# Kernel optimization log

Hardware: AMD Instinct MI355X
Metric: run time of the kernel (lower is better)

Reference implementation:

```python
import jax, jax.numpy as jnp
import numpy as np

N_NODES = 50000
N_EDGES = 800000
D_MODEL = 128
N_HEADS = 8
HEAD_DIM = D_MODEL // N_HEADS
SCALE = 1.0 / np.sqrt(HEAD_DIM)


def _linear_params(key, d_in, d_out):
    kw, kb = jax.random.split(key)
    bound = 1.0 / np.sqrt(d_in)
    W = jax.random.uniform(kw, (d_in, d_out), jnp.float32, -bound, bound)
    b = jax.random.uniform(kb, (d_out,), jnp.float32, -bound, bound)
    return W, b


def setup_inputs() -> dict:
    key = jax.random.key(0)
    ks = jax.random.split(key, 8)
    node_features = jax.random.normal(ks[0], (N_NODES, D_MODEL), jnp.float32)
    edge_index = jax.random.randint(ks[1], (2, N_EDGES), 0, N_NODES, jnp.int64 if jax.config.jax_enable_x64 else jnp.int32)
    edge_features = jax.random.normal(ks[2], (N_EDGES, D_MODEL), jnp.float32)
    Wq, bq = _linear_params(ks[3], D_MODEL, D_MODEL)
    Wk, bk = _linear_params(ks[4], D_MODEL, D_MODEL)
    Wv, bv = _linear_params(ks[5], D_MODEL, D_MODEL)
    We, be = _linear_params(ks[6], D_MODEL, N_HEADS)
    Wo, bo = _linear_params(ks[7], D_MODEL, D_MODEL)
    return {"node_features": node_features, "edge_index": edge_index,
            "edge_features": edge_features,
            "Wq": Wq, "bq": bq, "Wk": Wk, "bk": bk, "Wv": Wv, "bv": bv,
            "We": We, "be": be, "Wo": Wo, "bo": bo}


def reference(node_features, edge_index, edge_features,
              Wq, bq, Wk, bk, Wv, bv, We, be, Wo, bo):
    N = node_features.shape[0]
    Q = (node_features @ Wq + bq).reshape(N, N_HEADS, HEAD_DIM)
    K = (node_features @ Wk + bk).reshape(N, N_HEADS, HEAD_DIM)
    V = (node_features @ Wv + bv).reshape(N, N_HEADS, HEAD_DIM)
    row, col = edge_index[0], edge_index[1]
    # edge scores: [E, H]
    scores = jnp.einsum('ehd,ehd->eh', Q[row], K[col]) * SCALE
    scores = scores + (edge_features @ We + be)
    # segment softmax over destination node (row), per head
    seg_max = jax.ops.segment_max(scores, row, num_segments=N)          # [N, H]
    seg_max = jnp.where(jnp.isfinite(seg_max), seg_max, 0.0)
    ex = jnp.exp(scores - seg_max[row])                                  # [E, H]
    denom = jax.ops.segment_sum(ex, row, num_segments=N)                 # [N, H]
    att = ex / denom[row]
    # weighted aggregate of neighbor values: [N, H, D]
    out = jax.ops.segment_sum(att[:, :, None] * V[col], row, num_segments=N)
    out = out.reshape(N, D_MODEL)
    return out @ Wo + bo
```

## Files before the change

### kernel.cpp

```cpp
#include <hip/hip_runtime.h>
#include <hip/hip_bf16.h>
#include <math.h>

#define NNODES 50000
#define NEDGES 800000
#define DMODEL 128
#define QK_SCALE 0.25f
#define NSB 196

typedef float fvec4 __attribute__((ext_vector_type(4)));
typedef short sv8  __attribute__((ext_vector_type(8)));

__device__ __forceinline__ unsigned short f2bf(float f) {
    unsigned int u = __float_as_uint(f);
    unsigned int r = (u + 0x7FFFu + ((u >> 16) & 1u)) >> 16;
    return (unsigned short)r;
}

__device__ __forceinline__ void bf8_to_f32(uint4 u, fvec4& lo, fvec4& hi) {
    lo.x = __uint_as_float(u.x << 16); lo.y = __uint_as_float(u.x & 0xFFFF0000u);
    lo.z = __uint_as_float(u.y << 16); lo.w = __uint_as_float(u.y & 0xFFFF0000u);
    hi.x = __uint_as_float(u.z << 16); hi.y = __uint_as_float(u.z & 0xFFFF0000u);
    hi.z = __uint_as_float(u.w << 16); hi.w = __uint_as_float(u.w & 0xFFFF0000u);
}

__global__ __launch_bounds__(256) void prep_kernel(const float* __restrict__ X,
                                                   const float* __restrict__ Wq,
                                                   const float* __restrict__ Wk,
                                                   const float* __restrict__ Wv,
                                                   const float* __restrict__ Wo,
                                                   unsigned short* __restrict__ Xb,
                                                   unsigned short* __restrict__ Wb,
                                                   int* __restrict__ cnt) {
    int i = blockIdx.x * 256 + threadIdx.x;
    if (i < NNODES * 32) {
        float4 v = *(const float4*)&X[(size_t)i * 4];
        ushort4 s;
        s.x = f2bf(v.x); s.y = f2bf(v.y); s.z = f2bf(v.z); s.w = f2bf(v.w);
        *(ushort4*)&Xb[(size_t)i * 4] = s;
    } else {
        int j = i - NNODES * 32;
        if (j < 4 * 16384) {
            int w = j >> 14, rem = j & 16383;
            int n = rem >> 7, k = rem & 127;
            const float* src = (w == 0) ? Wq : (w == 1) ? Wk : (w == 2) ? Wv : Wo;
            Wb[j] = f2bf(src[k * 128 + n]);
        } else {
            int c = j - 4 * 16384;
            if (c < NNODES) cnt[c] = 0;
        }
    }
}

__global__ __launch_bounds__(256) void gemm_qkv(const unsigned short* __restrict__ Xb,
                                                const unsigned short* __restrict__ Wb,
                                                const float* __restrict__ bq,
                                                const float* __restrict__ bk,
                                                const float* __restrict__ bv,
                                                unsigned short* __restrict__ Qb,
                                                unsigned short* __restrict__ KVb,
                                                int M) {
    __shared__ unsigned short Als[64 * 128];
    __shared__ unsigned short Bls[128 * 128];
    char* Ac = (char*)Als;
    char* Bc = (char*)Bls;

    int z = blockIdx.y;
    int r0 = blockIdx.x * 64;
    int tid = threadIdx.x;
    int wave = tid >> 6, lane = tid & 63;

    const char* Wsrc = (const char*)(Wb + (size_t)z * 16384);

    #pragma unroll
    for (int p = 0; p < 4; ++p) {
        int o = p * 4096 + tid * 16;
        int r = o >> 8;
        int gr = r0 + r; if (gr >= M) gr = M - 1;
        uint4 v = *(const uint4*)((const char*)Xb + (size_t)gr * 256 + (o & 255));
        *(uint4*)(Ac + r * 256 + ((o & 255) ^ ((r & 7) << 4))) = v;
    }
    #pragma unroll
    for (int p = 0; p < 8; ++p) {
        int o = p * 4096 + tid * 16;
        int r = o >> 8;
        uint4 v = *(const uint4*)(Wsrc + o);
        *(uint4*)(Bc + (o ^ ((r & 7) << 4))) = v;
    }
    __syncthreads();

    fvec4 acc[8] = {};
    int arow = wave * 16 + (lane & 15);
    int kchunk = (lane >> 4) * 16;

    #pragma unroll
    for (int ks = 0; ks < 4; ++ks) {
        int ain = (ks * 64 + kchunk) ^ ((arow & 7) << 4);
        sv8 af = *(const sv8*)(Ac + arow * 256 + ain);
        #pragma unroll
        for (int cf = 0; cf < 8; ++cf) {
            int brow = cf * 16 + (lane & 15);
            int bin = (ks * 64 + kchunk) ^ ((brow & 7) << 4);
            sv8 bf = *(const sv8*)(Bc + brow * 256 + bin);
            acc[cf] = __builtin_amdgcn_mfma_f32_16x16x32_bf16(af, bf, acc[cf], 0, 0, 0);
        }
    }

    const float* bias = (z == 0) ? bq : (z == 1) ? bk : bv;

    #pragma unroll
    for (int cf = 0; cf < 8; ++cf) {
        int col = cf * 16 + (lane & 15);
        float b = bias[col];
        #pragma unroll
        for (int r = 0; r < 4; ++r) {
            int gr = r0 + wave * 16 + ((lane >> 4) * 4) + r;
            if (gr < M) {
                unsigned short val = f2bf(acc[cf][r] + b);
                if (z == 0) {
                    Qb[(size_t)gr * 128 + col] = val;
                } else {
                    int coff = (z == 1) ? 0 : 128;
                    int off = coff + ((col & 8) << 3) + ((col >> 4) << 3) + (col & 7);
                    KVb[(size_t)gr * 256 + off] = val;
                }
            }
        }
    }
}

__global__ __launch_bounds__(256) void gemm_out(const unsigned short* __restrict__ Ab,
                                                const unsigned short* __restrict__ Wob,
                                                const float* __restrict__ bo,
                                                float* __restrict__ outp, int M) {
    __shared__ unsigned short Als[64 * 128];
    __shared__ unsigned short Bls[128 * 128];
    char* Ac = (char*)Als;
    char* Bc = (char*)Bls;

    int r0 = blockIdx.x * 64;
    int tid = threadIdx.x;
    int wave = tid >> 6, lane = tid & 63;

    #pragma unroll
    for (int p = 0; p < 4; ++p) {
        int o = p * 4096 + tid * 16;
        int r = o >> 8;
        int gr = r0 + r; if (gr >= M) gr = M - 1;
        uint4 v = *(const uint4*)((const char*)Ab + (size_t)gr * 256 + (o & 255));
        *(uint4*)(Ac + r * 256 + ((o & 255) ^ ((r & 7) << 4))) = v;
    }
    #pragma unroll
    for (int p = 0; p < 8; ++p) {
        int o = p * 4096 + tid * 16;
        int r = o >> 8;
        uint4 v = *(const uint4*)((const char*)Wob + o);
        *(uint4*)(Bc + (o ^ ((r & 7) << 4))) = v;
    }
    __syncthreads();

    fvec4 acc[8] = {};
    int arow = wave * 16 + (lane & 15);
    int kchunk = (lane >> 4) * 16;

    #pragma unroll
    for (int ks = 0; ks < 4; ++ks) {
        int ain = (ks * 64 + kchunk) ^ ((arow & 7) << 4);
        sv8 af = *(const sv8*)(Ac + arow * 256 + ain);
        #pragma unroll
        for (int cf = 0; cf < 8; ++cf) {
            int brow = cf * 16 + (lane & 15);
            int bin = (ks * 64 + kchunk) ^ ((brow & 7) << 4);
            sv8 bf = *(const sv8*)(Bc + brow * 256 + bin);
            acc[cf] = __builtin_amdgcn_mfma_f32_16x16x32_bf16(af, bf, acc[cf], 0, 0, 0);
        }
    }

    #pragma unroll
    for (int cf = 0; cf < 8; ++cf) {
        int col = cf * 16 + (lane & 15);
        float b = bo[col];
        #pragma unroll
        for (int r = 0; r < 4; ++r) {
            int gr = r0 + wave * 16 + ((lane >> 4) * 4) + r;
            if (gr < M) outp[(size_t)gr * 128 + col] = acc[cf][r] + b;
        }
    }
}

__global__ __launch_bounds__(256) void hist_kernel(const int* __restrict__ row,
                                                   int* __restrict__ cnt) {
    int e = blockIdx.x * 256 + threadIdx.x;
    if (e < NEDGES) atomicAdd(&cnt[row[e]], 1);
}

__global__ __launch_bounds__(256) void scan1_kernel(const int* __restrict__ cnt,
                                                    int* __restrict__ bsum) {
    __shared__ int red[256];
    int idx = blockIdx.x * 256 + threadIdx.x;
    red[threadIdx.x] = (idx < NNODES) ? cnt[idx] : 0;
    __syncthreads();
    for (int off = 128; off > 0; off >>= 1) {
        if (threadIdx.x < off) red[threadIdx.x] += red[threadIdx.x + off];
        __syncthreads();
    }
    if (threadIdx.x == 0) bsum[blockIdx.x] = red[0];
}

__global__ __launch_bounds__(256) void scan2_kernel(const int* __restrict__ bsum,
                                                    int* __restrict__ bpre) {
    __shared__ int ps[256];
    int t = threadIdx.x;
    int v = (t < NSB) ? bsum[t] : 0;
    ps[t] = v;
    __syncthreads();
    for (int off = 1; off < 256; off <<= 1) {
        int x = (t >= off) ? ps[t - off] : 0;
        __syncthreads();
        ps[t] += x;
        __syncthreads();
    }
    if (t < NSB) bpre[t] = ps[t] - v;
}

__global__ __launch_bounds__(256) void scan3_kernel(const int* __restrict__ cnt,
                                                    const int* __restrict__ bpre,
                                                    int* __restrict__ offs,
                                                    int* __restrict__ cursor) {
    __shared__ int ps[256];
    int t = threadIdx.x;
    int idx = blockIdx.x * 256 + t;
    int v = (idx < NNODES) ? cnt[idx] : 0;
    ps[t] = v;
    __syncthreads();
    for (int off = 1; off < 256; off <<= 1) {
        int x = (t >= off) ? ps[t - off] : 0;
        __syncthreads();
        ps[t] += x;
        __syncthreads();
    }
    int ex = ps[t] - v + bpre[blockIdx.x];
    if (idx < NNODES) { offs[idx] = ex; cursor[idx] = ex; }
    if (idx == NNODES) offs[NNODES] = NEDGES;
}

__global__ __launch_bounds__(256) void ef_bias_scatter(const float* __restrict__ EF,
                                                       const int* __restrict__ row,
                                                       const int* __restrict__ col,
                                                       int* __restrict__ cursor,
                                                       const float* __restrict__ We,
                                                       const float* __restrict__ be,
                                                       unsigned short* __restrict__ ebias,
                                                       int* __restrict__ col_perm) {
    __shared__ float sWe[8][128];
    __shared__ float sbe[8];
    for (int i = threadIdx.x; i < 1024; i += 256) {
        int d = i >> 3, h = i & 7;
        sWe[h][d] = We[i];
    }
    if (threadIdx.x < 8) sbe[threadIdx.x] = be[threadIdx.x];
    __syncthreads();

    int g = blockIdx.x * 256 + threadIdx.x;
    int e = g >> 3;
    int s = g & 7;
    if (e >= NEDGES) return;
    int lane = threadIdx.x & 63;

    int pos = 0;
    if (s == 0) {
        int r = row[e];
        pos = atomicAdd(&cursor[r], 1);
        col_perm[pos] = col[e];
    }

    const fvec4* efv = (const fvec4*)(EF + (size_t)e * 128);
    float acc[8] = {0.f, 0.f, 0.f, 0.f, 0.f, 0.f, 0.f, 0.f};
    #pragma unroll
    for (int i = 0; i < 4; ++i) {
        int d4 = s + 8 * i;
        fvec4 v = __builtin_nontemporal_load(&efv[d4]);
        #pragma unroll
        for (int h = 0; h < 8; ++h) {
            fvec4 w = *(const fvec4*)&sWe[h][d4 * 4];
            acc[h] += v.x * w.x + v.y * w.y + v.z * w.z + v.w * w.w;
        }
    }

    #pragma unroll
    for (int off = 1; off < 8; off <<= 1)
        #pragma unroll
        for (int h = 0; h < 8; ++h)
            acc[h] += __shfl_xor(acc[h], off);

    pos = __shfl(pos, lane & ~7);
    ebias[(size_t)pos * 8 + s] = f2bf(acc[s] + sbe[s]);
}

__global__ __launch_bounds__(256) void fused_agg(const unsigned short* __restrict__ Qb,
                                                 const unsigned short* __restrict__ KV,
                                                 const unsigned short* __restrict__ ebias,
                                                 const int* __restrict__ col_perm,
                                                 const int* __restrict__ offs,
                                                 unsigned short* __restrict__ aggb) {
    int node = blockIdx.x * 4 + (threadIdx.x >> 6);
    if (node >= NNODES) return;
    int lane = threadIdx.x & 63;
    int slot = lane >> 3;
    int h    = lane & 7;
    int start = offs[node];
    int end   = offs[node + 1];

    const uint4* qp = (const uint4*)(Qb + (size_t)node * 128 + h * 16);
    uint4 qu0 = qp[0], qu1 = qp[1];
    fvec4 q0, q1, q2, q3;
    bf8_to_f32(qu0, q0, q1);
    bf8_to_f32(qu1, q2, q3);

    float m = -3.0e38f;
    float sum = 0.0f;
    fvec4 a0 = {0.f,0.f,0.f,0.f}, a1 = {0.f,0.f,0.f,0.f};
    fvec4 a2 = {0.f,0.f,0.f,0.f}, a3 = {0.f,0.f,0.f,0.f};

    for (int i = start + slot; i < end; i += 8) {
        int c = col_perm[i];
        float eb = __uint_as_float(((unsigned int)ebias[(size_t)i * 8 + h]) << 16);
        const uint4* kp = (const uint4*)(KV + (size_t)c * 256);
        uint4 ku0 = kp[h],      ku1 = kp[8 + h];
        uint4 vu0 = kp[16 + h], vu1 = kp[24 + h];
        fvec4 k0, k1, k2, k3, v0, v1, v2, v3;
        bf8_to_f32(ku0, k0, k1);
        bf8_to_f32(ku1, k2, k3);
        bf8_to_f32(vu0, v0, v1);
        bf8_to_f32(vu1, v2, v3);

        fvec4 d4 = q0 * k0 + q1 * k1 + q2 * k2 + q3 * k3;
        float dot = d4.x + d4.y + d4.z + d4.w;

        float s = dot * QK_SCALE + eb;
        float mn = fmaxf(m, s);
        float corr = __expf(m - mn);
        float w = __expf(s - mn);
        sum = sum * corr + w;
        a0 = a0 * corr + w * v0;
        a1 = a1 * corr + w * v1;
        a2 = a2 * corr + w * v2;
        a3 = a3 * corr + w * v3;
        m = mn;
    }

    #pragma unroll
    for (int off = 8; off < 64; off <<= 1) {
        float mo = __shfl_xor(m, off);
        float so = __shfl_xor(sum, off);
        fvec4 b0, b1, b2, b3;
        b0.x = __shfl_xor(a0.x, off); b0.y = __shfl_xor(a0.y, off);
        b0.z = __shfl_xor(a0.z, off); b0.w = __shfl_xor(a0.w, off);
        b1.x = __shfl_xor(a1.x, off); b1.y = __shfl_xor(a1.y, off);
        b1.z = __shfl_xor(a1.z, off); b1.w = __shfl_xor(a1.w, off);
        b2.x = __shfl_xor(a2.x, off); b2.y = __shfl_xor(a2.y, off);
        b2.z = __shfl_xor(a2.z, off); b2.w = __shfl_xor(a2.w, off);
        b3.x = __shfl_xor(a3.x, off); b3.y = __shfl_xor(a3.y, off);
        b3.z = __shfl_xor(a3.z, off); b3.w = __shfl_xor(a3.w, off);
        float M = fmaxf(m, mo);
        float c1 = __expf(m - M);
        float c2 = __expf(mo - M);
        sum = sum * c1 + so * c2;
        a0 = a0 * c1 + b0 * c2;
        a1 = a1 * c1 + b1 * c2;
        a2 = a2 * c1 + b2 * c2;
        a3 = a3 * c1 + b3 * c2;
        m = M;
    }

    if (slot == 0) {
        float inv = (sum > 0.0f) ? (1.0f / sum) : 0.0f;
        unsigned short* op = aggb + (size_t)node * 128 + h * 16;
        ushort4 s;
        s.x = f2bf(a0.x * inv); s.y = f2bf(a0.y * inv); s.z = f2bf(a0.z * inv); s.w = f2bf(a0.w * inv);
        *(ushort4*)(op + 0) = s;
        s.x = f2bf(a1.x * inv); s.y = f2bf(a1.y * inv); s.z = f2bf(a1.z * inv); s.w = f2bf(a1.w * inv);
        *(ushort4*)(op + 4) = s;
        s.x = f2bf(a2.x * inv); s.y = f2bf(a2.y * inv); s.z = f2bf(a2.z * inv); s.w = f2bf(a2.w * inv);
        *(ushort4*)(op + 8) = s;
        s.x = f2bf(a3.x * inv); s.y = f2bf(a3.y * inv); s.z = f2bf(a3.z * inv); s.w = f2bf(a3.w * inv);
        *(ushort4*)(op + 12) = s;
    }
}

extern "C" void kernel_launch(void* const* d_in, const int* in_sizes, int n_in,
                              void* d_out, int out_size, void* d_ws, size_t ws_size,
                              hipStream_t stream) {
    const float* node = (const float*)d_in[0];
    const int*   ei   = (const int*)d_in[1];
    const float* ef   = (const float*)d_in[2];
    const float* Wq   = (const float*)d_in[3];
    const float* bq   = (const float*)d_in[4];
    const float* Wk   = (const float*)d_in[5];
    const float* bk   = (const float*)d_in[6];
    const float* Wv   = (const float*)d_in[7];
    const float* bv   = (const float*)d_in[8];
    const float* We   = (const float*)d_in[9];
    const float* be   = (const float*)d_in[10];
    const float* Wo   = (const float*)d_in[11];
    const float* bo   = (const float*)d_in[12];
    float* out = (float*)d_out;

    const int* row = ei;
    const int* col = ei + NEDGES;

    unsigned short* Qb   = (unsigned short*)d_ws;
    unsigned short* KVb  = Qb  + (size_t)NNODES * 128;
    unsigned short* Xb   = KVb + (size_t)NNODES * 256;
    unsigned short* Wb   = Xb  + (size_t)NNODES * 128;
    unsigned short* aggb = Wb  + 4 * 16384;
    unsigned short* ebb  = aggb + (size_t)NNODES * 128;
    int*   cnt      = (int*)(ebb + (size_t)NEDGES * 8);
    int*   offs     = cnt + NNODES;
    int*   cursor   = offs + NNODES + 1;
    int*   col_perm = cursor + NNODES;
    int*   bsum     = col_perm + NEDGES;
    int*   bpre     = bsum + 256;

    prep_kernel<<<(NNODES * 32 + 4 * 16384 + NNODES + 255) / 256, 256, 0, stream>>>(
        node, Wq, Wk, Wv, Wo, Xb, Wb, cnt);
    hist_kernel<<<(NEDGES + 255) / 256, 256, 0, stream>>>(row, cnt);
    scan1_kernel<<<NSB, 256, 0, stream>>>(cnt, bsum);
    scan2_kernel<<<1, 256, 0, stream>>>(bsum, bpre);
    scan3_kernel<<<NSB, 256, 0, stream>>>(cnt, bpre, offs, cursor);

    dim3 gqkv((NNODES + 63) / 64, 3);
    gemm_qkv<<<gqkv, 256, 0, stream>>>(Xb, Wb, bq, bk, bv, Qb, KVb, NNODES);

    ef_bias_scatter<<<NEDGES * 8 / 256, 256, 0, stream>>>(ef, row, col, cursor, We, be, ebb, col_perm);

    fused_agg<<<(NNODES + 3) / 4, 256, 0, stream>>>(Qb, KVb, ebb, col_perm, offs, aggb);

    gemm_out<<<(NNODES + 63) / 64, 256, 0, stream>>>(aggb, Wb + 3 * 16384, bo, out, NNODES);
}
```

Baseline: 310.3 us.

## Use one 8-lane group per node in aggregation and grid-stride edge-bias kernel

The aggregation kernel now assigns 8 lanes (one per head) to each node and walks that node's edges serially, instead of a 64-lane wavefront spreading edges over 8 slots. This drops the cross-slot online-softmax shuffle merge and packs the bf16 output into wider stores. The edge-bias kernel becomes a grid-stride loop with a fixed block count and keeps the We weights in registers, replacing the per-block shared-memory load. The cost is less parallelism per high-degree node, more divergence between the node groups sharing a wavefront, and higher register use in the edge-bias kernel.

```diff
diff --git a/kernel.cpp b/kernel.cpp
--- a/kernel.cpp
+++ b/kernel.cpp
@@ -7,6 +7,7 @@
 #define DMODEL 128
 #define QK_SCALE 0.25f
 #define NSB 196
+#define EFB_BLOCKS 2048
 
 typedef float fvec4 __attribute__((ext_vector_type(4)));
 typedef short sv8  __attribute__((ext_vector_type(8)));
@@ -15,6 +16,10 @@
     unsigned int u = __float_as_uint(f);
     unsigned int r = (u + 0x7FFFu + ((u >> 16) & 1u)) >> 16;
     return (unsigned short)r;
+}
+
+__device__ __forceinline__ unsigned int pack2bf(float lo, float hi) {
+    return (unsigned int)f2bf(lo) | ((unsigned int)f2bf(hi) << 16);
 }
 
 __device__ __forceinline__ void bf8_to_f32(uint4 u, fvec4& lo, fvec4& hi) {
@@ -252,49 +257,56 @@
                                                        const float* __restrict__ be,
                                                        unsigned short* __restrict__ ebias,
                                                        int* __restrict__ col_perm) {
-    __shared__ float sWe[8][128];
-    __shared__ float sbe[8];
-    for (int i = threadIdx.x; i < 1024; i += 256) {
-        int d = i >> 3, h = i & 7;
-        sWe[h][d] = We[i];
-    }
-    if (threadIdx.x < 8) sbe[threadIdx.x] = be[threadIdx.x];
-    __syncthreads();
-
-    int g = blockIdx.x * 256 + threadIdx.x;
-    int e = g >> 3;
-    int s = g & 7;
-    if (e >= NEDGES) return;
     int lane = threadIdx.x & 63;
-
-    int pos = 0;
-    if (s == 0) {
-        int r = row[e];
-        pos = atomicAdd(&cursor[r], 1);
-        col_perm[pos] = col[e];
-    }
-
-    const fvec4* efv = (const fvec4*)(EF + (size_t)e * 128);
-    float acc[8] = {0.f, 0.f, 0.f, 0.f, 0.f, 0.f, 0.f, 0.f};
-    #pragma unroll
-    for (int i = 0; i < 4; ++i) {
-        int d4 = s + 8 * i;
-        fvec4 v = __builtin_nontemporal_load(&efv[d4]);
-        #pragma unroll
-        for (int h = 0; h < 8; ++h) {
-            fvec4 w = *(const fvec4*)&sWe[h][d4 * 4];
-            acc[h] += v.x * w.x + v.y * w.y + v.z * w.z + v.w * w.w;
-        }
-    }
-
-    #pragma unroll
-    for (int off = 1; off < 8; off <<= 1)
-        #pragma unroll
-        for (int h = 0; h < 8; ++h)
-            acc[h] += __shfl_xor(acc[h], off);
-
-    pos = __shfl(pos, lane & ~7);
-    ebias[(size_t)pos * 8 + s] = f2bf(acc[s] + sbe[s]);
+    int s = lane & 7;
+
+    fvec4 wlo[4][4], whi[4][4];
+    #pragma unroll
+    for (int i = 0; i < 4; ++i)
+        #pragma unroll
+        for (int c = 0; c < 4; ++c) {
+            const fvec4* wp = (const fvec4*)(We + ((size_t)(4 * (s + 8 * i) + c)) * 8);
+            wlo[i][c] = wp[0];
+            whi[i][c] = wp[1];
+        }
+    float be_s = be[s];
+
+    long long stride = (long long)gridDim.x * 256;
+    for (long long g = (long long)blockIdx.x * 256 + threadIdx.x;
+         g < (long long)NEDGES * 8; g += stride) {
+        int e = (int)(g >> 3);
+
+        int pos = 0;
+        if (s == 0) {
+            int r = row[e];
+            pos = atomicAdd(&cursor[r], 1);
+            col_perm[pos] = col[e];
+        }
+
+        const fvec4* efv = (const fvec4*)(EF + (size_t)e * 128);
+        fvec4 aclo = {0.f, 0.f, 0.f, 0.f}, achi = {0.f, 0.f, 0.f, 0.f};
+        #pragma unroll
+        for (int i = 0; i < 4; ++i) {
+            fvec4 v = __builtin_nontemporal_load(&efv[s + 8 * i]);
+            aclo += v.x * wlo[i][0] + v.y * wlo[i][1] + v.z * wlo[i][2] + v.w * wlo[i][3];
+            achi += v.x * whi[i][0] + v.y * whi[i][1] + v.z * whi[i][2] + v.w * whi[i][3];
+        }
+
+        float a0 = aclo.x, a1 = aclo.y, a2 = aclo.z, a3 = aclo.w;
+        float a4 = achi.x, a5 = achi.y, a6 = achi.z, a7 = achi.w;
+        #pragma unroll
+        for (int off = 1; off < 8; off <<= 1) {
+            a0 += __shfl_xor(a0, off); a1 += __shfl_xor(a1, off);
+            a2 += __shfl_xor(a2, off); a3 += __shfl_xor(a3, off);
+            a4 += __shfl_xor(a4, off); a5 += __shfl_xor(a5, off);
+            a6 += __shfl_xor(a6, off); a7 += __shfl_xor(a7, off);
+        }
+        float r = (s < 4) ? ((s < 2) ? (s == 0 ? a0 : a1) : (s == 2 ? a2 : a3))
+                          : ((s < 6) ? (s == 4 ? a4 : a5) : (s == 6 ? a6 : a7));
+
+        pos = __shfl(pos, lane & ~7);
+        ebias[(size_t)pos * 8 + s] = f2bf(r + be_s);
+    }
 }
 
 __global__ __launch_bounds__(256) void fused_agg(const unsigned short* __restrict__ Qb,
@@ -303,11 +315,10 @@
                                                  const int* __restrict__ col_perm,
                                                  const int* __restrict__ offs,
                                                  unsigned short* __restrict__ aggb) {
-    int node = blockIdx.x * 4 + (threadIdx.x >> 6);
+    int node = blockIdx.x * 32 + (threadIdx.x >> 3);
     if (node >= NNODES) return;
-    int lane = threadIdx.x & 63;
-    int slot = lane >> 3;
-    int h    = lane & 7;
+    int h = threadIdx.x & 7;
+
     int start = offs[node];
     int end   = offs[node + 1];
 
@@ -322,7 +333,7 @@
     fvec4 a0 = {0.f,0.f,0.f,0.f}, a1 = {0.f,0.f,0.f,0.f};
     fvec4 a2 = {0.f,0.f,0.f,0.f}, a3 = {0.f,0.f,0.f,0.f};
 
-    for (int i = start + slot; i < end; i += 8) {
+    for (int i = start; i < end; ++i) {
         int c = col_perm[i];
         float eb = __uint_as_float(((unsigned int)ebias[(size_t)i * 8 + h]) << 16);
         const uint4* kp = (const uint4*)(KV + (size_t)c * 256);
@@ -349,43 +360,19 @@
         m = mn;
     }
 
-    #pragma unroll
-    for (int off = 8; off < 64; off <<= 1) {
-        float mo = __shfl_xor(m, off);
-        float so = __shfl_xor(sum, off);
-        fvec4 b0, b1, b2, b3;
-        b0.x = __shfl_xor(a0.x, off); b0.y = __shfl_xor(a0.y, off);
-        b0.z = __shfl_xor(a0.z, off); b0.w = __shfl_xor(a0.w, off);
-        b1.x = __shfl_xor(a1.x, off); b1.y = __shfl_xor(a1.y, off);
-        b1.z = __shfl_xor(a1.z, off); b1.w = __shfl_xor(a1.w, off);
-        b2.x = __shfl_xor(a2.x, off); b2.y = __shfl_xor(a2.y, off);
-        b2.z = __shfl_xor(a2.z, off); b2.w = __shfl_xor(a2.w, off);
-        b3.x = __shfl_xor(a3.x, off); b3.y = __shfl_xor(a3.y, off);
-        b3.z = __shfl_xor(a3.z, off); b3.w = __shfl_xor(a3.w, off);
-        float M = fmaxf(m, mo);
-        float c1 = __expf(m - M);
-        float c2 = __expf(mo - M);
-        sum = sum * c1 + so * c2;
-        a0 = a0 * c1 + b0 * c2;
-        a1 = a1 * c1 + b1 * c2;
-        a2 = a2 * c1 + b2 * c2;
-        a3 = a3 * c1 + b3 * c2;
-        m = M;
-    }
-
-    if (slot == 0) {
-        float inv = (sum > 0.0f) ? (1.0f / sum) : 0.0f;
-        unsigned short* op = aggb + (size_t)node * 128 + h * 16;
-        ushort4 s;
-        s.x = f2bf(a0.x * inv); s.y = f2bf(a0.y * inv); s.z = f2bf(a0.z * inv); s.w = f2bf(a0.w * inv);
-        *(ushort4*)(op + 0) = s;
-        s.x = f2bf(a1.x * inv); s.y = f2bf(a1.y * inv); s.z = f2bf(a1.z * inv); s.w = f2bf(a1.w * inv);
-        *(ushort4*)(op + 4) = s;
-        s.x = f2bf(a2.x * inv); s.y = f2bf(a2.y * inv); s.z = f2bf(a2.z * inv); s.w = f2bf(a2.w * inv);
-        *(ushort4*)(op + 8) = s;
-        s.x = f2bf(a3.x * inv); s.y = f2bf(a3.y * inv); s.z = f2bf(a3.z * inv); s.w = f2bf(a3.w * inv);
-        *(ushort4*)(op + 12) = s;
-    }
+    float inv = (sum > 0.0f) ? (1.0f / sum) : 0.0f;
+    unsigned short* op = aggb + (size_t)node * 128 + h * 16;
+    uint4 o1, o2;
+    o1.x = pack2bf(a0.x * inv, a0.y * inv);
+    o1.y = pack2bf(a0.z * inv, a0.w * inv);
+    o1.z = pack2bf(a1.x * inv, a1.y * inv);
+    o1.w = pack2bf(a1.z * inv, a1.w * inv);
+    o2.x = pack2bf(a2.x * inv, a2.y * inv);
+    o2.y = pack2bf(a2.z * inv, a2.w * inv);
+    o2.z = pack2bf(a3.x * inv, a3.y * inv);
+    o2.w = pack2bf(a3.z * inv, a3.w * inv);
+    *(uint4*)(op) = o1;
+    *(uint4*)(op + 8) = o2;
 }
 
 extern "C" void kernel_launch(void* const* d_in, const int* in_sizes, int n_in,
@@ -432,9 +419,9 @@
     dim3 gqkv((NNODES + 63) / 64, 3);
     gemm_qkv<<<gqkv, 256, 0, stream>>>(Xb, Wb, bq, bk, bv, Qb, KVb, NNODES);
 
-    ef_bias_scatter<<<NEDGES * 8 / 256, 256, 0, stream>>>(ef, row, col, cursor, We, be, ebb, col_perm);
-
-    fused_agg<<<(NNODES + 3) / 4, 256, 0, stream>>>(Qb, KVb, ebb, col_perm, offs, aggb);
+    ef_bias_scatter<<<EFB_BLOCKS, 256, 0, stream>>>(ef, row, col, cursor, We, be, ebb, col_perm);
+
+    fused_agg<<<(NNODES + 31) / 32, 256, 0, stream>>>(Qb, KVb, ebb, col_perm, offs, aggb);
 
     gemm_out<<<(NNODES + 63) / 64, 256, 0, stream>>>(aggb, Wb + 3 * 16384, bo, out, NNODES);
 }
```

Result: slower. 372.2 us (+19.9%).
